# Kernel optimization log

Hardware: AMD Instinct MI355X
Metric: run time of the kernel (lower is better)

## Reference

```python
import jax, jax.numpy as jnp
import numpy as np

D = 256      # d_model (module-level constant in source)
H = 4        # num_heads
HD = D // H  # head dim = 64
B = 16
T = 512
STEP = 0.5   # self.step_size
NEG = -1e9
SCALE = 1.0 / np.sqrt(HD).astype(np.float32)


def _ln(x, g, b):
    m = jnp.mean(x, -1, keepdims=True)
    v = jnp.var(x, -1, keepdims=True)
    return (x - m) / jnp.sqrt(v + 1e-5) * g + b


def _forward(x, h0,
             sa_wq, sa_wk, sa_wv, sa_wo, sa_bq, sa_bk, sa_bv, sa_bo,
             f_w1, f_b1, f_w2, f_b2,
             ta_wq, ta_wk, ta_wv, ta_wo, ta_bq, ta_bk, ta_bv, ta_bo,
             tr_w1, tr_b1, tr_w2, tr_b2,
             ps_w, ps_b, sp_w, sp_b,
             ln1_g, ln1_b, ln2_g, ln2_b, ln3_g, ln3_b, ln4_g, ln4_b):
    Bz, Tz, Dz = x.shape
    # ---- causal self-attention over parallel_repr ----
    q = (x @ sa_wq + sa_bq).reshape(Bz, Tz, H, HD)
    k = (x @ sa_wk + sa_bk).reshape(Bz, Tz, H, HD)
    v = (x @ sa_wv + sa_bv).reshape(Bz, Tz, H, HD)
    scores = jnp.einsum('bqhd,bkhd->bhqk', q, k) * SCALE
    causal = jnp.tril(jnp.ones((Tz, Tz), bool))
    scores = jnp.where(causal, scores, NEG)
    attn = jnp.einsum('bhqk,bkhd->bqhd', jax.nn.softmax(scores, -1), v)
    attn = attn.reshape(Bz, Tz, Dz) @ sa_wo + sa_bo
    x = _ln(x + attn, ln1_g, ln1_b)
    # ---- FFN with sequential guidance ----
    guid = h0 @ sp_w + sp_b                      # sequential_to_parallel, [B, D]
    ffn_in = x + 0.3 * guid[:, None, :]
    ffn = jax.nn.gelu(ffn_in @ f_w1 + f_b1, approximate=False) @ f_w2 + f_b2
    x = _ln(x + ffn, ln2_g, ln2_b)
    # ---- sequential scan with growing-cache trajectory attention ----
    # past states only enter through their K/V projections, so project each
    # new state once when it is appended (same math as re-projecting the cache).
    def step(carry, inp):
        h, kbuf, vbuf = carry                    # kbuf/vbuf: [T, B, H, HD]
        t, xt = inp                              # xt: [B, D]
        qt = (xt @ ta_wq + ta_bq).reshape(Bz, H, HD)
        sc = jnp.einsum('bhd,tbhd->bht', qt, kbuf) * SCALE
        valid = (jnp.arange(Tz) < t)[None, None, :]
        ctx = jnp.einsum('bht,tbhd->bhd',
                         jax.nn.softmax(jnp.where(valid, sc, NEG), -1), vbuf)
        ctx = ctx.reshape(Bz, Dz) @ ta_wo + ta_bo
        ctx = jnp.where(t > 0, ctx, 0.0)         # torch code zeroes context at t=0
        pg = xt @ ps_w + ps_b                    # parallel_to_sequential
        comb = jnp.concatenate([xt + 0.3 * pg, ctx], -1)
        delta = jax.nn.gelu(comb @ tr_w1 + tr_b1, approximate=False) @ tr_w2 + tr_b2
        h = _ln(h + STEP * delta, ln3_g, ln3_b)
        kbuf = kbuf.at[t].set((h @ ta_wk + ta_bk).reshape(Bz, H, HD))
        vbuf = vbuf.at[t].set((h @ ta_wv + ta_bv).reshape(Bz, H, HD))
        return (h, kbuf, vbuf), None

    buf0 = jnp.zeros((Tz, Bz, H, HD), x.dtype)
    (hT, _, _), _ = jax.lax.scan(step, (h0, buf0, buf0),
                                 (jnp.arange(Tz), jnp.swapaxes(x, 0, 1)))
    return x, _ln(hT, ln4_g, ln4_b)


def setup_inputs() -> dict:
    ks = iter(jax.random.split(jax.random.key(0), 64))
    def w(*shape):
        return jax.random.normal(next(ks), shape, jnp.float32) * 0.02
    inp = {
        'x': jax.random.normal(next(ks), (B, T, D), jnp.float32),
        'h0': jax.random.normal(next(ks), (B, D), jnp.float32),
        'sa_wq': w(D, D), 'sa_wk': w(D, D), 'sa_wv': w(D, D), 'sa_wo': w(D, D),
        'sa_bq': w(D), 'sa_bk': w(D), 'sa_bv': w(D), 'sa_bo': w(D),
        'f_w1': w(D, 4 * D), 'f_b1': w(4 * D), 'f_w2': w(4 * D, D), 'f_b2': w(D),
        'ta_wq': w(D, D), 'ta_wk': w(D, D), 'ta_wv': w(D, D), 'ta_wo': w(D, D),
        'ta_bq': w(D), 'ta_bk': w(D), 'ta_bv': w(D), 'ta_bo': w(D),
        'tr_w1': w(2 * D, 2 * D), 'tr_b1': w(2 * D), 'tr_w2': w(2 * D, D), 'tr_b2': w(D),
        'ps_w': w(D, D), 'ps_b': w(D), 'sp_w': w(D, D), 'sp_b': w(D),
        'ln1_g': jnp.ones(D), 'ln1_b': jnp.zeros(D),
        'ln2_g': jnp.ones(D), 'ln2_b': jnp.zeros(D),
        'ln3_g': jnp.ones(D), 'ln3_b': jnp.zeros(D),
        'ln4_g': jnp.ones(D), 'ln4_b': jnp.zeros(D),
    }
    return inp


def reference(x, h0,
              sa_wq, sa_wk, sa_wv, sa_wo, sa_bq, sa_bk, sa_bv, sa_bo,
              f_w1, f_b1, f_w2, f_b2,
              ta_wq, ta_wk, ta_wv, ta_wo, ta_bq, ta_bk, ta_bv, ta_bo,
              tr_w1, tr_b1, tr_w2, tr_b2,
              ps_w, ps_b, sp_w, sp_b,
              ln1_g, ln1_b, ln2_g, ln2_b, ln3_g, ln3_b, ln4_g, ln4_b):
    return _forward(x, h0,
                    sa_wq, sa_wk, sa_wv, sa_wo, sa_bq, sa_bk, sa_bv, sa_bo,
                    f_w1, f_b1, f_w2, f_b2,
                    ta_wq, ta_wk, ta_wv, ta_wo, ta_bq, ta_bk, ta_bv, ta_bo,
                    tr_w1, tr_b1, tr_w2, tr_b2,
                    ps_w, ps_b, sp_w, sp_b,
                    ln1_g, ln1_b, ln2_g, ln2_b, ln3_g, ln3_b, ln4_g, ln4_b)
```

## Files before the change

kernel.cpp:

```cpp
#include <hip/hip_runtime.h>
#include <hip/hip_bf16.h>

typedef __bf16 bf16x8 __attribute__((ext_vector_type(8)));
typedef float f32x4 __attribute__((ext_vector_type(4)));

__device__ __forceinline__ float b2f(ushort u){
  union { uint u; float f; } x; x.u = ((uint)u) << 16; return x.f;
}
__device__ __forceinline__ ushort f2b(float f){
  union { float f; uint u; } x; x.f = f;
  uint r = x.u + 0x7fff + ((x.u >> 16) & 1);
  return (ushort)(r >> 16);
}
__device__ __forceinline__ uint pack_bf2(float a, float b){
  return (uint)f2b(a) | ((uint)f2b(b) << 16);
}
__device__ __forceinline__ float lo16(uint u){ union{uint a;float f;}x; x.a=u<<16; return x.f; }
__device__ __forceinline__ float hi16(uint u){ union{uint a;float f;}x; x.a=u&0xffff0000u; return x.f; }
__device__ __forceinline__ float gelu_exact(float v){
  return 0.5f * v * (1.0f + erff(v * 0.70710678118654752f));
}

template<int AF32, int ACT>
__global__ __launch_bounds__(256) void gemm_kernel(
    const void* __restrict__ Av, const float* __restrict__ W, int ldw,
    const float* __restrict__ bias, const float* residf,
    float* Cf, ushort* Cb,
    int M, int N, int K, float scale)
{
  __shared__ __align__(16) ushort Al[64*40];
  __shared__ __align__(16) ushort Bl[64*40];
  const int nb = N >> 6;
  const int rb = blockIdx.x / nb, cb = blockIdx.x % nb;
  const int tid = threadIdx.x;
  const int w = tid >> 6, l = tid & 63;
  f32x4 acc[4];
#pragma unroll
  for(int i=0;i<4;i++) acc[i] = (f32x4){0.f,0.f,0.f,0.f};
  const int ar = tid >> 2, ai = (tid & 3) << 3;
  const int bk = tid >> 3, bn = (tid & 7) << 3;
  for(int kb = 0; kb < K; kb += 32){
    uint4 au;
    if(AF32){
      const float* Ap = (const float*)Av + (size_t)(rb*64 + ar)*K + kb + ai;
      float4 f0 = *(const float4*)Ap;
      float4 f1 = *(const float4*)(Ap + 4);
      au.x = pack_bf2(f0.x,f0.y); au.y = pack_bf2(f0.z,f0.w);
      au.z = pack_bf2(f1.x,f1.y); au.w = pack_bf2(f1.z,f1.w);
    } else {
      au = *(const uint4*)((const ushort*)Av + (size_t)(rb*64 + ar)*K + kb + ai);
    }
    const float* Wp = W + (size_t)(kb + bk)*ldw + cb*64 + bn;
    float4 w0 = *(const float4*)Wp;
    float4 w1 = *(const float4*)(Wp + 4);
    ushort bs[8];
    bs[0]=f2b(w0.x); bs[1]=f2b(w0.y); bs[2]=f2b(w0.z); bs[3]=f2b(w0.w);
    bs[4]=f2b(w1.x); bs[5]=f2b(w1.y); bs[6]=f2b(w1.z); bs[7]=f2b(w1.w);
    __syncthreads();
    *(uint4*)&Al[ar*40 + ai] = au;
#pragma unroll
    for(int i=0;i<8;i++) Bl[(bn+i)*40 + bk] = bs[i];
    __syncthreads();
    bf16x8 af = *(const bf16x8*)&Al[(w*16 + (l&15))*40 + (l>>4)*8];
#pragma unroll
    for(int c4=0;c4<4;c4++){
      bf16x8 bfv = *(const bf16x8*)&Bl[(c4*16 + (l&15))*40 + (l>>4)*8];
      acc[c4] = __builtin_amdgcn_mfma_f32_16x16x32_bf16(af, bfv, acc[c4], 0,0,0);
    }
  }
#pragma unroll
  for(int c4=0;c4<4;c4++){
#pragma unroll
    for(int r=0;r<4;r++){
      int row = rb*64 + w*16 + (l>>4)*4 + r;
      int col = cb*64 + c4*16 + (l&15);
      size_t idx = (size_t)row*N + col;
      float vv = acc[c4][r];
      if(bias) vv += bias[col];
      vv *= scale;
      if(residf) vv += residf[idx];
      if(ACT) vv = gelu_exact(vv);
      if(Cf) Cf[idx] = vv;
      if(Cb) Cb[idx] = f2b(vv);
    }
  }
}

__global__ __launch_bounds__(256) void attn_kernel(const ushort* __restrict__ Q,
    const ushort* __restrict__ K, const ushort* __restrict__ V, ushort* __restrict__ O)
{
  __shared__ float s[16*520];
  __shared__ float kt[64*66];
  __shared__ float rowm[16], rowr[16], redx[256];
  const int bid = blockIdx.x;
  const int qb = bid & 31, h = (bid>>5)&3, b = bid>>7;
  const int tid = threadIdx.x;
  const int qi = tid >> 4, jj = tid & 15;
  const int qrow = qb*16 + qi;
  float qreg[64];
  {
    const ushort* qp = Q + ((size_t)(b*512 + qrow))*256 + h*64;
#pragma unroll
    for(int d=0; d<64; d++) qreg[d] = b2f(qp[d])*0.125f;
  }
  const int ntile = (qb*16 + 79) >> 6;
  for(int jt=0; jt<ntile; jt++){
    {
      int jr = tid >> 2, d0 = (tid & 3) << 4;
      const ushort* kp = K + ((size_t)(b*512 + jt*64 + jr))*256 + h*64 + d0;
#pragma unroll
      for(int i=0;i<16;i++) kt[jr*66 + d0 + i] = b2f(kp[i]);
    }
    __syncthreads();
#pragma unroll
    for(int jl=0;jl<4;jl++){
      int jloc = jj*4 + jl;
      int j = jt*64 + jloc;
      float a = 0.f;
#pragma unroll
      for(int d=0; d<64; d++) a += qreg[d]*kt[jloc*66 + d];
      s[qi*520 + j] = (j <= qrow) ? a : -1e30f;
    }
    __syncthreads();
  }
  const int nj = ntile*64;
  float m = -1e30f;
  for(int j=jj; j<nj; j+=16) m = fmaxf(m, s[qi*520 + j]);
  redx[jj*16 + qi] = m;
  __syncthreads();
  if(tid < 16){
    float mm = -1e30f;
#pragma unroll
    for(int k2=0;k2<16;k2++) mm = fmaxf(mm, redx[k2*16 + tid]);
    rowm[tid] = mm;
  }
  __syncthreads();
  float mrow = rowm[qi];
  float ssum = 0.f;
  for(int j=jj; j<nj; j+=16){
    float e = __expf(s[qi*520+j] - mrow);
    s[qi*520+j] = e; ssum += e;
  }
  redx[jj*16 + qi] = ssum;
  __syncthreads();
  if(tid < 16){
    float t2 = 0.f;
#pragma unroll
    for(int k2=0;k2<16;k2++) t2 += redx[k2*16 + tid];
    rowr[tid] = 1.0f/t2;
  }
  const int dd = jj;
  float acc4[4] = {0,0,0,0};
  for(int jt=0; jt<ntile; jt++){
    __syncthreads();
    {
      int jr = tid >> 2, d0 = (tid & 3) << 4;
      const ushort* vp = V + ((size_t)(b*512 + jt*64 + jr))*256 + h*64 + d0;
#pragma unroll
      for(int i=0;i<16;i++) kt[jr*66 + d0 + i] = b2f(vp[i]);
    }
    __syncthreads();
#pragma unroll
    for(int jl=0;jl<64;jl++){
      float p = s[qi*520 + jt*64 + jl];
#pragma unroll
      for(int i=0;i<4;i++) acc4[i] += p*kt[jl*66 + dd*4 + i];
    }
  }
  float rr = rowr[qi];
  ushort* op = O + ((size_t)(b*512 + qrow))*256 + h*64 + dd*4;
#pragma unroll
  for(int i=0;i<4;i++) op[i] = f2b(acc4[i]*rr);
}

__global__ __launch_bounds__(256) void ln_kernel(const float* __restrict__ in,
    const float* __restrict__ g, const float* __restrict__ be,
    float* outf, ushort* outb)
{
  int row = blockIdx.x*4 + (threadIdx.x>>6);
  int lane = threadIdx.x & 63;
  size_t idx = (size_t)row*256 + lane*4;
  float4 v = *(const float4*)(in + idx);
  float s1 = v.x+v.y+v.z+v.w;
  float s2 = v.x*v.x + v.y*v.y + v.z*v.z + v.w*v.w;
#pragma unroll
  for(int off=32; off; off>>=1){ s1 += __shfl_xor(s1,off); s2 += __shfl_xor(s2,off); }
  float mu = s1*(1.f/256.f);
  float var = s2*(1.f/256.f) - mu*mu;
  float r = rsqrtf(var + 1e-5f);
  float vals[4] = {v.x,v.y,v.z,v.w};
  float4 o4; ushort4 ob;
  float* oo = (float*)&o4; ushort* obp = (ushort*)&ob;
#pragma unroll
  for(int i=0;i<4;i++){
    int d = lane*4 + i;
    float y = (vals[i]-mu)*r*g[d] + be[d];
    oo[i] = y; obp[i] = f2b(y);
  }
  if(outf) *(float4*)(outf+idx) = o4;
  if(outb) *(ushort4*)(outb+idx) = ob;
}

__global__ void guid_kernel(const float* __restrict__ h0, const float* __restrict__ spw,
                            const float* __restrict__ spb, float* __restrict__ guid)
{
  int b = blockIdx.x, c = threadIdx.x;
  float s = spb[c];
  for(int r=0;r<256;r++) s += h0[b*256+r]*spw[r*256+c];
  guid[b*256+c] = s;
}

__global__ void ffnin_kernel(const float* __restrict__ x1, const float* __restrict__ guid,
                             ushort* __restrict__ out)
{
  size_t base = ((size_t)blockIdx.x*256 + threadIdx.x)*8;
  int row = (int)(base >> 8); int bb = row >> 9; int c = (int)(base & 255);
  float4 v0 = *(const float4*)(x1 + base);
  float4 v1 = *(const float4*)(x1 + base + 4);
  const float* gp = guid + bb*256 + c;
  const float* xs = (const float*)&v0;
  ushort o[8];
#pragma unroll
  for(int i=0;i<4;i++) o[i] = f2b(xs[i] + 0.3f*gp[i]);
  const float* xs1 = (const float*)&v1;
#pragma unroll
  for(int i=0;i<4;i++) o[4+i] = f2b(xs1[i] + 0.3f*gp[4+i]);
  *(uint4*)(out + base) = *(uint4*)o;
}

__global__ void bo_kernel(const float* __restrict__ ta_bo, const float* __restrict__ tr_w1,
                          float* __restrict__ bo_f)
{
  int c = threadIdx.x;
  float s = 0.f;
  for(int m=0;m<256;m++) s += ta_bo[m]*tr_w1[(size_t)(256+m)*512 + c];
  bo_f[c] = s;
}

__global__ __launch_bounds__(512, 1) void scan_kernel(
    const ushort* __restrict__ qtb, const ushort* __restrict__ Ubf,
    const float* __restrict__ Wf, const float* __restrict__ bo_f,
    float* cbuf, float* dbuf, int* flags,
    const float* __restrict__ ta_wk, const float* __restrict__ ta_wv,
    const float* __restrict__ ta_bk, const float* __restrict__ ta_bv,
    const float* __restrict__ tr_w2, const float* __restrict__ tr_b2,
    const float* __restrict__ ln3_g, const float* __restrict__ ln3_b,
    const float* __restrict__ ln4_g, const float* __restrict__ ln4_b,
    const float* __restrict__ h0, float* __restrict__ out_h)
{
  __shared__ __align__(16) float red[2][1024];
  __shared__ __align__(16) float pbuf[512];
  __shared__ __align__(16) float hbuf[256];
  __shared__ __align__(16) float ctxL[256];
  __shared__ __align__(16) float qbufS[2][64];
  __shared__ float mG[2][16], sG[2][16];
  __shared__ __align__(16) float numS[2][64];
  __shared__ float mzS[2][2];
  __shared__ float sLastP[4];
  __shared__ __align__(16) float glbuf[128];
  __shared__ int cp_same[4];
  extern __shared__ __align__(16) ushort dynL[];
  ushort* kcL = dynL;
  ushort* vcL = dynL + 512*66;

  const int tid = threadIdx.x;
  const int bid = blockIdx.x;
  const int b = bid & 15;
  const int role = bid >> 4;
  const int b4 = b*4;
  const int w8 = tid >> 6;

  if(role < 4){
    for(int i = tid; i < 512*66; i += 512){ kcL[i] = 0; vcL[i] = 0; }
  }

  int myxcc;
  asm volatile("s_getreg_b32 %0, hwreg(HW_REG_XCC_ID)" : "=s"(myxcc));
  if(tid == 0)
    __hip_atomic_store(&flags[256 + bid], myxcc + 1, __ATOMIC_RELEASE, __HIP_MEMORY_SCOPE_AGENT);
  if(tid < 4){
    int cbid = (role < 4) ? (64 + tid*16 + b) : (tid*16 + b);
    int v;
    while((v = __hip_atomic_load(&flags[256 + cbid], __ATOMIC_ACQUIRE, __HIP_MEMORY_SCOPE_AGENT)) == 0)
      __builtin_amdgcn_s_sleep(8);
    cp_same[tid] = ((v - 1) == myxcc);
  }
  __syncthreads();
  const int anyrem = !(cp_same[0] && cp_same[1] && cp_same[2] && cp_same[3]);

  if(role < 4){
    const int hd = role;
    const int bh = b4 + hd;
    const int out = tid >> 2, sX = tid & 3;
    const int kvSel = out >> 6, colX = out & 63;
    const float* WX = kvSel ? ta_wv : ta_wk;
    uint wp[32];
#pragma unroll
    for(int i=0;i<32;i++){
      int r0 = 8*i + 2*sX;
      wp[i] = pack_bf2(WX[(size_t)r0*256 + hd*64 + colX],
                       WX[(size_t)(r0+1)*256 + hd*64 + colX]);
    }
    const float pbX = kvSel ? ta_bv[hd*64 + colX] : ta_bk[hd*64 + colX];
    float h4[4], b2r4[4], g34[4], b34[4];
    if(tid < 64){
#pragma unroll
      for(int c=0;c<4;c++){
        int d = 4*tid + c;
        h4[c] = h0[b*256 + d]; b2r4[c] = tr_b2[d]; g34[c] = ln3_g[d]; b34[c] = ln3_b[d];
      }
      *(float4*)&hbuf[4*tid] = *(float4*)h4;
    }
    const int j_sh = (tid >= 64) ? (tid - 64) : (448 + tid);
    const int gsh = j_sh >> 5;
    const int lsh = tid & 31;
    __syncthreads();

    ushort qpre = 0;
    if(tid >= 448) qpre = qtb[((size_t)(b*512 + 1))*256 + hd*64 + (tid - 448)];

#pragma clang loop unroll(disable)
    for(int t=0;t<512;t++){
      if(tid >= 448){
        qbufS[(t+1)&1][tid-448] = b2f(qpre)*0.125f;
        int tq = (t+2 < 512) ? (t+2) : 511;
        qpre = qtb[((size_t)(b*512 + tq))*256 + hd*64 + (tid - 448)];
      }
      if(t > 0){
        float acc = 0.f;
#pragma unroll
        for(int i=0;i<32;i++){
          float2 hv = *(const float2*)&hbuf[8*i + 2*sX];
          acc += hv.x*lo16(wp[i]) + hv.y*hi16(wp[i]);
        }
        acc += __shfl_xor(acc, 1);
        acc += __shfl_xor(acc, 2);
        float kf = acc + pbX;
        if(sX == 0){
          ushort u = f2b(kf);
          if(kvSel == 0) kcL[(t-1)*66 + colX] = u;
          else           vcL[(t-1)*66 + colX] = u;
        }
        float pv = (kvSel == 0 && sX == 0) ? qbufS[t&1][colX]*kf : 0.f;
        pv += __shfl_xor(pv, 4);
        pv += __shfl_xor(pv, 8);
        pv += __shfl_xor(pv, 16);
        pv += __shfl_xor(pv, 32);
        if(tid < 256 && (tid & 63) == 0) sLastP[tid >> 6] = pv;
        __syncthreads();
        if(tid < 64){
          const int par = t & 1;
          float sl = (sLastP[0] + sLastP[1]) + (sLastP[2] + sLastP[3]);
          float mo = mzS[par][0], Zo = mzS[par][1];
          float m = fmaxf(mo, sl);
          float so = __expf(mo - m);
          float el = __expf(sl - m);
          float Z = Zo*so + el;
          float vlast = b2f(vcL[(t-1)*66 + tid]);
          cbuf[b*256 + hd*64 + tid] = (numS[par][tid]*so + el*vlast) / Z;
          asm volatile("s_waitcnt vmcnt(0)" ::: "memory");
          if(tid == 0){
            *(volatile int*)&flags[bh] = t;
            if(anyrem)
              __hip_atomic_store(&flags[128 + bh], t, __ATOMIC_RELEASE, __HIP_MEMORY_SCOPE_AGENT);
          }
        }
      }

      {
        const int par = (t+1)&1;
        float s = -3.0e38f;
        if(j_sh < t){
          const uint* kr = (const uint*)(kcL + j_sh*66);
          const float* qS = qbufS[par];
          float a = 0.f;
#pragma unroll
          for(int w=0; w<32; w++){
            uint kk = kr[w];
            float2 q2 = *(const float2*)&qS[2*w];
            a += q2.x*lo16(kk) + q2.y*hi16(kk);
          }
          s = a;
        }
        float gm = s;
#pragma unroll
        for(int off=16; off; off>>=1) gm = fmaxf(gm, __shfl_xor(gm, off));
        float e = (j_sh < t) ? __expf(s - gm) : 0.f;
        pbuf[j_sh] = e;
        float gs = e;
#pragma unroll
        for(int off=16; off; off>>=1) gs += __shfl_xor(gs, off);
        if(lsh == 0){ mG[par][gsh] = gm; sG[par][gsh] = gs; }
        int nn = t - gsh*32; nn = nn < 0 ? 0 : (nn > 32 ? 32 : nn);
        float a0 = 0.f, a1 = 0.f;
        const uint* vbase = (const uint*)vcL;
#pragma unroll 4
        for(int i=0;i<nn;i++){
          int j2 = gsh*32 + i;
          uint vv = vbase[j2*33 + lsh];
          float p = pbuf[j2];
          a0 += p*lo16(vv); a1 += p*hi16(vv);
        }
        float2 pr; pr.x = a0; pr.y = a1;
        *(float2*)&red[par][gsh*64 + 2*lsh] = pr;
      }
      __syncthreads();
      if(tid < 64){
        const int par = (t+1)&1;
        float mo = mG[par][0];
#pragma unroll
        for(int g=1; g<16; g++) mo = fmaxf(mo, mG[par][g]);
        float Zo = 0.f, nm = 0.f;
#pragma unroll
        for(int g=0; g<16; g++){
          float scl = __expf(mG[par][g] - mo);
          Zo += sG[par][g]*scl;
          nm += red[par][g*64 + tid]*scl;
        }
        numS[par][tid] = nm;
        if(tid == 0){ mzS[par][0] = mo; mzS[par][1] = Zo; }
      }
      if(tid < 32){
        const int sh = tid >> 3, wv = tid & 7;
        if(cp_same[sh]){
          while(*(volatile int*)&flags[512 + (b4+sh)*8 + wv] < t+1) __builtin_amdgcn_s_sleep(1);
        } else {
          while(__hip_atomic_load(&flags[1024 + (b4+sh)*8 + wv], __ATOMIC_RELAXED, __HIP_MEMORY_SCOPE_AGENT) < t+1)
            __builtin_amdgcn_s_sleep(2);
        }
      }
      if(tid < 64){
        if(anyrem) __builtin_amdgcn_fence(__ATOMIC_ACQUIRE, "agent");
        float ds[4] = {0.f,0.f,0.f,0.f};
#pragma unroll
        for(int i=0;i<4;i++){
          const float* dp = &dbuf[(b4+i)*256 + 4*tid];
#pragma unroll
          for(int c=0;c<4;c++)
            ds[c] += __hip_atomic_load(dp + c, __ATOMIC_RELAXED, __HIP_MEMORY_SCOPE_AGENT);
        }
        float v4[4]; float s1 = 0.f, s2 = 0.f;
#pragma unroll
        for(int c=0;c<4;c++){
          v4[c] = h4[c] + 0.5f*(ds[c] + b2r4[c]);
          s1 += v4[c]; s2 += v4[c]*v4[c];
        }
#pragma unroll
        for(int off=32; off; off>>=1){ s1 += __shfl_xor(s1,off); s2 += __shfl_xor(s2,off); }
        float mu = s1*(1.f/256.f);
        float qq = s2*(1.f/256.f) - mu*mu;
        float rstd = rsqrtf(qq + 1e-5f);
#pragma unroll
        for(int c=0;c<4;c++) h4[c] = (v4[c]-mu)*rstd*g34[c] + b34[c];
        *(float4*)&hbuf[4*tid] = *(float4*)h4;
      }
      __syncthreads();
    }

    if(hd == 0 && tid < 64){
      float s1 = 0.f, s2 = 0.f;
#pragma unroll
      for(int c=0;c<4;c++){ s1 += h4[c]; s2 += h4[c]*h4[c]; }
#pragma unroll
      for(int off=32; off; off>>=1){ s1 += __shfl_xor(s1,off); s2 += __shfl_xor(s2,off); }
      float mu = s1*(1.f/256.f);
      float qq = s2*(1.f/256.f) - mu*mu;
      float rstd = rsqrtf(qq + 1e-5f);
#pragma unroll
      for(int c=0;c<4;c++){
        int d = 4*tid + c;
        out_h[b*256 + d] = (h4[c]-mu)*rstd*ln4_g[d] + ln4_b[d];
      }
    }
  } else {
    const int ish = role - 4;
    const int hid = tid >> 2, sY = tid & 3;
    const int colY = ish*128 + hid;
    uint wfp[32];
#pragma unroll
    for(int i=0;i<32;i++){
      int r0 = 8*i + 2*sY;
      wfp[i] = pack_bf2(Wf[(size_t)r0*512 + colY], Wf[(size_t)(r0+1)*512 + colY]);
    }
    const int dcol = tid >> 1, s2 = tid & 1;
    uint w2p[32];
#pragma unroll
    for(int i=0;i<32;i++){
      int r0 = ish*128 + 4*i + 2*s2;
      w2p[i] = pack_bf2(tr_w2[(size_t)r0*256 + dcol], tr_w2[(size_t)(r0+1)*256 + dcol]);
    }
    const float borr = (sY==0) ? bo_f[colY] : 0.f;
    __syncthreads();

#pragma clang loop unroll(disable)
    for(int t=0;t<512;t++){
      ushort uvs = 0;
      if(sY == 0) uvs = Ubf[((size_t)(b*512 + t))*512 + colY];
      if(t > 0){
        if(tid < 256){
          int q = tid >> 6;
          if(cp_same[q]){
            while(*(volatile int*)&flags[b4 + q] < t) __builtin_amdgcn_s_sleep(1);
          } else {
            while(__hip_atomic_load(&flags[128 + b4 + q], __ATOMIC_RELAXED, __HIP_MEMORY_SCOPE_AGENT) < t)
              __builtin_amdgcn_s_sleep(2);
          }
        }
        if(anyrem) __builtin_amdgcn_fence(__ATOMIC_ACQUIRE, "agent");
        if(tid < 256) ctxL[tid] = *(volatile float*)&cbuf[b*256 + tid];
      }
      __syncthreads();
      float accf = 0.f;
      if(t > 0){
#pragma unroll
        for(int i=0;i<32;i++){
          float2 c2 = *(const float2*)&ctxL[8*i + 2*sY];
          accf += c2.x*lo16(wfp[i]) + c2.y*hi16(wfp[i]);
        }
        accf += __shfl_xor(accf, 1);
        accf += __shfl_xor(accf, 2);
      }
      if(sY == 0){
        float g1 = b2f(uvs) + ((t>0) ? (borr + accf) : 0.f);
        glbuf[hid] = gelu_exact(g1);
      }
      __syncthreads();
      {
        float dp = 0.f;
#pragma unroll
        for(int i=0;i<32;i++){
          float2 gv = *(const float2*)&glbuf[4*i + 2*s2];
          dp += gv.x*lo16(w2p[i]) + gv.y*hi16(w2p[i]);
        }
        dp += __shfl_xor(dp, 1);
        if(s2 == 0) dbuf[(b4+ish)*256 + dcol] = dp;
      }
      asm volatile("s_waitcnt vmcnt(0)" ::: "memory");
      if((tid & 63) == 0){
        *(volatile int*)&flags[512 + (b4+ish)*8 + w8] = t+1;
        if(anyrem)
          __hip_atomic_store(&flags[1024 + (b4+ish)*8 + w8], t+1, __ATOMIC_RELEASE, __HIP_MEMORY_SCOPE_AGENT);
      }
    }
  }
}

#define OFF_FLAGS ((size_t)0)
#define OFF_BOF   ((size_t)8192)
#define OFF_CBUF  ((size_t)16384)
#define OFF_DBUF  ((size_t)32768)
#define OFF_GUID  ((size_t)98304)
#define OFF_WF    ((size_t)131072)
#define OFF_Z1    ((size_t)(1u<<20))
#define OFF_Z2    ((size_t)(5u<<20))
#define OFF_Z3    ((size_t)(9u<<20))
#define OFF_Z4    ((size_t)(13u<<20))
#define OFF_M     ((size_t)(17u<<20))

#define SCAN_DYN_LDS (512*66*2*2)

extern "C" void kernel_launch(void* const* d_in, const int* in_sizes, int n_in,
                              void* d_out, int out_size, void* d_ws, size_t ws_size,
                              hipStream_t stream)
{
  const float* x     = (const float*)d_in[0];
  const float* h0    = (const float*)d_in[1];
  const float* sa_wq = (const float*)d_in[2];
  const float* sa_wk = (const float*)d_in[3];
  const float* sa_wv = (const float*)d_in[4];
  const float* sa_wo = (const float*)d_in[5];
  const float* sa_bq = (const float*)d_in[6];
  const float* sa_bk = (const float*)d_in[7];
  const float* sa_bv = (const float*)d_in[8];
  const float* sa_bo = (const float*)d_in[9];
  const float* f_w1  = (const float*)d_in[10];
  const float* f_b1  = (const float*)d_in[11];
  const float* f_w2  = (const float*)d_in[12];
  const float* f_b2  = (const float*)d_in[13];
  const float* ta_wq = (const float*)d_in[14];
  const float* ta_wk = (const float*)d_in[15];
  const float* ta_wv = (const float*)d_in[16];
  const float* ta_wo = (const float*)d_in[17];
  const float* ta_bq = (const float*)d_in[18];
  const float* ta_bk = (const float*)d_in[19];
  const float* ta_bv = (const float*)d_in[20];
  const float* ta_bo = (const float*)d_in[21];
  const float* tr_w1 = (const float*)d_in[22];
  const float* tr_b1 = (const float*)d_in[23];
  const float* tr_w2 = (const float*)d_in[24];
  const float* tr_b2 = (const float*)d_in[25];
  const float* ps_w  = (const float*)d_in[26];
  const float* ps_b  = (const float*)d_in[27];
  const float* sp_w  = (const float*)d_in[28];
  const float* sp_b  = (const float*)d_in[29];
  const float* ln1_g = (const float*)d_in[30];
  const float* ln1_b = (const float*)d_in[31];
  const float* ln2_g = (const float*)d_in[32];
  const float* ln2_b = (const float*)d_in[33];
  const float* ln3_g = (const float*)d_in[34];
  const float* ln3_b = (const float*)d_in[35];
  const float* ln4_g = (const float*)d_in[36];
  const float* ln4_b = (const float*)d_in[37];

  char* ws = (char*)d_ws;
  int*    flags = (int*)   (ws + OFF_FLAGS);
  float*  bo_f  = (float*) (ws + OFF_BOF);
  float*  cbuf  = (float*) (ws + OFF_CBUF);
  float*  dbuf  = (float*) (ws + OFF_DBUF);
  float*  guid  = (float*) (ws + OFF_GUID);
  float*  Wff   = (float*) (ws + OFF_WF);
  ushort* qb    = (ushort*)(ws + OFF_Z1);
  ushort* kb    = (ushort*)(ws + OFF_Z2);
  ushort* vb    = (ushort*)(ws + OFF_Z3);
  ushort* attnb = (ushort*)(ws + OFF_Z4);
  float*  x0pre = (float*) (ws + OFF_Z1);
  float*  x1f   = (float*) (ws + OFF_Z3);
  ushort* ffnb  = (ushort*)(ws + OFF_M);
  ushort* mid   = (ushort*)(ws + OFF_M + (4u<<20));
  float*  x2pre = (float*) (ws + OFF_Z1);
  ushort* abf   = (ushort*)(ws + OFF_Z4);
  ushort* qtb   = (ushort*)(ws + OFF_Z3);
  ushort* Ubf   = (ushort*)(ws + OFF_M);
  float*  outb  = (float*)d_out;
  float*  out_h = outb + (out_size - 4096);

  static int attr_done = 0;
  if(!attr_done){
    hipFuncSetAttribute((const void*)scan_kernel,
                        hipFuncAttributeMaxDynamicSharedMemorySize, SCAN_DYN_LDS);
    attr_done = 1;
  }

  hipMemsetAsync(flags, 0, 8192, stream);

  gemm_kernel<1,0><<<512, 256, 0, stream>>>(x, sa_wq, 256, sa_bq, nullptr, nullptr, qb, 8192,256,256, 1.0f);
  gemm_kernel<1,0><<<512, 256, 0, stream>>>(x, sa_wk, 256, sa_bk, nullptr, nullptr, kb, 8192,256,256, 1.0f);
  gemm_kernel<1,0><<<512, 256, 0, stream>>>(x, sa_wv, 256, sa_bv, nullptr, nullptr, vb, 8192,256,256, 1.0f);
  attn_kernel<<<2048, 256, 0, stream>>>(qb, kb, vb, attnb);
  gemm_kernel<0,0><<<512, 256, 0, stream>>>(attnb, sa_wo, 256, sa_bo, x, x0pre, nullptr, 8192,256,256, 1.0f);
  ln_kernel<<<2048, 256, 0, stream>>>(x0pre, ln1_g, ln1_b, x1f, nullptr);
  guid_kernel<<<16, 256, 0, stream>>>(h0, sp_w, sp_b, guid);
  ffnin_kernel<<<1024, 256, 0, stream>>>(x1f, guid, ffnb);
  gemm_kernel<0,1><<<1024, 256, 0, stream>>>(ffnb, f_w1, 1024, f_b1, nullptr, nullptr, mid, 8192,512,256, 1.0f);
  gemm_kernel<0,0><<<512, 256, 0, stream>>>(mid, f_w2, 256, f_b2, x1f, x2pre, nullptr, 8192,256,512, 1.0f);
  gemm_kernel<0,1><<<1024, 256, 0, stream>>>(ffnb, f_w1 + 512, 1024, f_b1 + 512, nullptr, nullptr, mid, 8192,512,256, 1.0f);
  gemm_kernel<0,0><<<512, 256, 0, stream>>>(mid, f_w2 + (size_t)512*256, 256, nullptr, x2pre, x2pre, nullptr, 8192,256,512, 1.0f);
  ln_kernel<<<2048, 256, 0, stream>>>(x2pre, ln2_g, ln2_b, outb, nullptr);

  gemm_kernel<1,0><<<512, 256, 0, stream>>>(outb, ps_w, 256, ps_b, outb, nullptr, abf, 8192,256,256, 0.3f);
  gemm_kernel<0,0><<<1024, 256, 0, stream>>>(abf, tr_w1, 512, tr_b1, nullptr, nullptr, Ubf, 8192,512,256, 1.0f);
  gemm_kernel<1,0><<<512, 256, 0, stream>>>(outb, ta_wq, 256, ta_bq, nullptr, nullptr, qtb, 8192,256,256, 1.0f);
  gemm_kernel<1,0><<<32, 256, 0, stream>>>(ta_wo, tr_w1 + (size_t)256*512, 512, nullptr, nullptr, Wff, nullptr, 256,512,256, 1.0f);
  bo_kernel<<<1, 512, 0, stream>>>(ta_bo, tr_w1, bo_f);

  scan_kernel<<<128, 512, SCAN_DYN_LDS, stream>>>(qtb, Ubf, Wff, bo_f, cbuf, dbuf, flags,
                                                  ta_wk, ta_wv, ta_bk, ta_bv, tr_w2, tr_b2,
                                                  ln3_g, ln3_b, ln4_g, ln4_b, h0, out_h);
}
```

Before: 3.526 ms.

## Pack data with step tags to replace separate flag handshakes in scan

The cross-block handshakes in the sequential scan kernel are rebuilt. Each value now goes out as a 64-bit word holding the data and the step index as a float, so consumers poll the data itself instead of waiting on a separate flag and then reading the payload. This removes the vmcnt waits, the flag stores and the acquire fences from the per-step critical path. The dot-product loops are also split into four independent accumulators for more instruction-level parallelism. In exchange, the cbuf and dbuf buffers double in size, the memset grows, and correctness now depends on 64-bit stores being atomic.

```diff
diff --git a/kernel.cpp b/kernel.cpp
--- a/kernel.cpp
+++ b/kernel.cpp
@@ -20,6 +20,8 @@
 __device__ __forceinline__ float gelu_exact(float v){
   return 0.5f * v * (1.0f + erff(v * 0.70710678118654752f));
 }
+
+union U64F2 { unsigned long long u; float2 f; };
 
 template<int AF32, int ACT>
 __global__ __launch_bounds__(256) void gemm_kernel(
@@ -240,7 +242,7 @@
 __global__ __launch_bounds__(512, 1) void scan_kernel(
     const ushort* __restrict__ qtb, const ushort* __restrict__ Ubf,
     const float* __restrict__ Wf, const float* __restrict__ bo_f,
-    float* cbuf, float* dbuf, int* flags,
+    float2* cbuf, float2* dbuf, int* flags,
     const float* __restrict__ ta_wk, const float* __restrict__ ta_wv,
     const float* __restrict__ ta_bk, const float* __restrict__ ta_bv,
     const float* __restrict__ tr_w2, const float* __restrict__ tr_b2,
@@ -268,7 +270,6 @@
   const int b = bid & 15;
   const int role = bid >> 4;
   const int b4 = b*4;
-  const int w8 = tid >> 6;
 
   if(role < 4){
     for(int i = tid; i < 512*66; i += 512){ kcL[i] = 0; vcL[i] = 0; }
@@ -290,7 +291,6 @@
 
   if(role < 4){
     const int hd = role;
-    const int bh = b4 + hd;
     const int out = tid >> 2, sX = tid & 3;
     const int kvSel = out >> 6, colX = out & 63;
     const float* WX = kvSel ? ta_wv : ta_wk;
@@ -327,12 +327,19 @@
         qpre = qtb[((size_t)(b*512 + tq))*256 + hd*64 + (tid - 448)];
       }
       if(t > 0){
-        float acc = 0.f;
-#pragma unroll
-        for(int i=0;i<32;i++){
-          float2 hv = *(const float2*)&hbuf[8*i + 2*sX];
-          acc += hv.x*lo16(wp[i]) + hv.y*hi16(wp[i]);
-        }
+        float aa0=0.f, aa1=0.f, aa2=0.f, aa3=0.f;
+#pragma unroll
+        for(int i=0;i<32;i+=4){
+          float2 h0v = *(const float2*)&hbuf[8*i + 2*sX];
+          float2 h1v = *(const float2*)&hbuf[8*(i+1) + 2*sX];
+          float2 h2v = *(const float2*)&hbuf[8*(i+2) + 2*sX];
+          float2 h3v = *(const float2*)&hbuf[8*(i+3) + 2*sX];
+          aa0 += h0v.x*lo16(wp[i])   + h0v.y*hi16(wp[i]);
+          aa1 += h1v.x*lo16(wp[i+1]) + h1v.y*hi16(wp[i+1]);
+          aa2 += h2v.x*lo16(wp[i+2]) + h2v.y*hi16(wp[i+2]);
+          aa3 += h3v.x*lo16(wp[i+3]) + h3v.y*hi16(wp[i+3]);
+        }
+        float acc = (aa0+aa1)+(aa2+aa3);
         acc += __shfl_xor(acc, 1);
         acc += __shfl_xor(acc, 2);
         float kf = acc + pbX;
@@ -357,13 +364,10 @@
           float el = __expf(sl - m);
           float Z = Zo*so + el;
           float vlast = b2f(vcL[(t-1)*66 + tid]);
-          cbuf[b*256 + hd*64 + tid] = (numS[par][tid]*so + el*vlast) / Z;
-          asm volatile("s_waitcnt vmcnt(0)" ::: "memory");
-          if(tid == 0){
-            *(volatile int*)&flags[bh] = t;
-            if(anyrem)
-              __hip_atomic_store(&flags[128 + bh], t, __ATOMIC_RELEASE, __HIP_MEMORY_SCOPE_AGENT);
-          }
+          U64F2 st; st.f.x = (numS[par][tid]*so + el*vlast) / Z; st.f.y = (float)t;
+          unsigned long long* cp = (unsigned long long*)&cbuf[b*256 + hd*64 + tid];
+          if(!anyrem) *(volatile unsigned long long*)cp = st.u;
+          else __hip_atomic_store(cp, st.u, __ATOMIC_RELEASE, __HIP_MEMORY_SCOPE_AGENT);
         }
       }
 
@@ -373,14 +377,20 @@
         if(j_sh < t){
           const uint* kr = (const uint*)(kcL + j_sh*66);
           const float* qS = qbufS[par];
-          float a = 0.f;
-#pragma unroll
-          for(int w=0; w<32; w++){
-            uint kk = kr[w];
-            float2 q2 = *(const float2*)&qS[2*w];
-            a += q2.x*lo16(kk) + q2.y*hi16(kk);
+          float a0=0.f, a1=0.f, a2=0.f, a3=0.f;
+#pragma unroll
+          for(int w=0; w<32; w+=4){
+            uint k0 = kr[w], k1 = kr[w+1], k2 = kr[w+2], k3 = kr[w+3];
+            float2 q0 = *(const float2*)&qS[2*w];
+            float2 q1 = *(const float2*)&qS[2*(w+1)];
+            float2 q2 = *(const float2*)&qS[2*(w+2)];
+            float2 q3 = *(const float2*)&qS[2*(w+3)];
+            a0 += q0.x*lo16(k0) + q0.y*hi16(k0);
+            a1 += q1.x*lo16(k1) + q1.y*hi16(k1);
+            a2 += q2.x*lo16(k2) + q2.y*hi16(k2);
+            a3 += q3.x*lo16(k3) + q3.y*hi16(k3);
           }
-          s = a;
+          s = (a0+a1)+(a2+a3);
         }
         float gm = s;
 #pragma unroll
@@ -407,38 +417,59 @@
       __syncthreads();
       if(tid < 64){
         const int par = (t+1)&1;
-        float mo = mG[par][0];
-#pragma unroll
-        for(int g=1; g<16; g++) mo = fmaxf(mo, mG[par][g]);
-        float Zo = 0.f, nm = 0.f;
-#pragma unroll
-        for(int g=0; g<16; g++){
-          float scl = __expf(mG[par][g] - mo);
-          Zo += sG[par][g]*scl;
-          nm += red[par][g*64 + tid]*scl;
-        }
-        numS[par][tid] = nm;
-        if(tid == 0){ mzS[par][0] = mo; mzS[par][1] = Zo; }
-      }
-      if(tid < 32){
-        const int sh = tid >> 3, wv = tid & 7;
-        if(cp_same[sh]){
-          while(*(volatile int*)&flags[512 + (b4+sh)*8 + wv] < t+1) __builtin_amdgcn_s_sleep(1);
+        float m0 = mG[par][0], m1 = mG[par][1];
+#pragma unroll
+        for(int g=2; g<16; g+=2){ m0 = fmaxf(m0, mG[par][g]); m1 = fmaxf(m1, mG[par][g+1]); }
+        float mo = fmaxf(m0, m1);
+        float Zo0=0.f, Zo1=0.f, nm0=0.f, nm1=0.f;
+#pragma unroll
+        for(int g=0; g<16; g+=2){
+          float sc0 = __expf(mG[par][g] - mo);
+          float sc1 = __expf(mG[par][g+1] - mo);
+          Zo0 += sG[par][g]*sc0;   Zo1 += sG[par][g+1]*sc1;
+          nm0 += red[par][g*64 + tid]*sc0;
+          nm1 += red[par][(g+1)*64 + tid]*sc1;
+        }
+        numS[par][tid] = nm0 + nm1;
+        if(tid == 0){ mzS[par][0] = mo; mzS[par][1] = Zo0 + Zo1; }
+      }
+      if(tid < 64){
+        float ds[4] = {0.f,0.f,0.f,0.f};
+        const float want = (float)(t+1);
+        U64F2 xx[16];
+        if(!anyrem){
+          int ok;
+          do{
+            ok = 1;
+#pragma unroll
+            for(int i=0;i<4;i++)
+#pragma unroll
+              for(int c=0;c<4;c++)
+                xx[i*4+c].u = *(volatile unsigned long long*)&dbuf[(b4+i)*256 + 4*tid + c];
+#pragma unroll
+            for(int k2=0;k2<16;k2++) ok &= (xx[k2].f.y == want);
+          } while(!ok);
         } else {
-          while(__hip_atomic_load(&flags[1024 + (b4+sh)*8 + wv], __ATOMIC_RELAXED, __HIP_MEMORY_SCOPE_AGENT) < t+1)
-            __builtin_amdgcn_s_sleep(2);
-        }
-      }
-      if(tid < 64){
-        if(anyrem) __builtin_amdgcn_fence(__ATOMIC_ACQUIRE, "agent");
-        float ds[4] = {0.f,0.f,0.f,0.f};
-#pragma unroll
-        for(int i=0;i<4;i++){
-          const float* dp = &dbuf[(b4+i)*256 + 4*tid];
-#pragma unroll
-          for(int c=0;c<4;c++)
-            ds[c] += __hip_atomic_load(dp + c, __ATOMIC_RELAXED, __HIP_MEMORY_SCOPE_AGENT);
-        }
+          int ok;
+          do{
+            ok = 1;
+#pragma unroll
+            for(int i=0;i<4;i++)
+#pragma unroll
+              for(int c=0;c<4;c++){
+                unsigned long long* pp = (unsigned long long*)&dbuf[(b4+i)*256 + 4*tid + c];
+                xx[i*4+c].u = cp_same[i] ? *(volatile unsigned long long*)pp
+                    : __hip_atomic_load(pp, __ATOMIC_RELAXED, __HIP_MEMORY_SCOPE_AGENT);
+              }
+#pragma unroll
+            for(int k2=0;k2<16;k2++) ok &= (xx[k2].f.y == want);
+            if(!ok) __builtin_amdgcn_s_sleep(1);
+          } while(!ok);
+        }
+#pragma unroll
+        for(int i=0;i<4;i++)
+#pragma unroll
+          for(int c=0;c<4;c++) ds[c] += xx[i*4+c].f.x;
         float v4[4]; float s1 = 0.f, s2 = 0.f;
 #pragma unroll
         for(int c=0;c<4;c++){
@@ -498,25 +529,38 @@
       if(sY == 0) uvs = Ubf[((size_t)(b*512 + t))*512 + colY];
       if(t > 0){
         if(tid < 256){
-          int q = tid >> 6;
+          const int q = tid >> 6;
+          unsigned long long* sp = (unsigned long long*)&cbuf[b*256 + tid];
+          U64F2 x;
+          const float tf = (float)t;
           if(cp_same[q]){
-            while(*(volatile int*)&flags[b4 + q] < t) __builtin_amdgcn_s_sleep(1);
+            do { x.u = *(volatile unsigned long long*)sp; } while(x.f.y != tf);
           } else {
-            while(__hip_atomic_load(&flags[128 + b4 + q], __ATOMIC_RELAXED, __HIP_MEMORY_SCOPE_AGENT) < t)
-              __builtin_amdgcn_s_sleep(2);
+            for(;;){
+              x.u = __hip_atomic_load(sp, __ATOMIC_RELAXED, __HIP_MEMORY_SCOPE_AGENT);
+              if(x.f.y == tf) break;
+              __builtin_amdgcn_s_sleep(1);
+            }
           }
-        }
-        if(anyrem) __builtin_amdgcn_fence(__ATOMIC_ACQUIRE, "agent");
-        if(tid < 256) ctxL[tid] = *(volatile float*)&cbuf[b*256 + tid];
+          ctxL[tid] = x.f.x;
+        }
       }
       __syncthreads();
       float accf = 0.f;
       if(t > 0){
-#pragma unroll
-        for(int i=0;i<32;i++){
-          float2 c2 = *(const float2*)&ctxL[8*i + 2*sY];
-          accf += c2.x*lo16(wfp[i]) + c2.y*hi16(wfp[i]);
-        }
+        float aa0=0.f, aa1=0.f, aa2=0.f, aa3=0.f;
+#pragma unroll
+        for(int i=0;i<32;i+=4){
+          float2 c0 = *(const float2*)&ctxL[8*i + 2*sY];
+          float2 c1 = *(const float2*)&ctxL[8*(i+1) + 2*sY];
+          float2 c2 = *(const float2*)&ctxL[8*(i+2) + 2*sY];
+          float2 c3 = *(const float2*)&ctxL[8*(i+3) + 2*sY];
+          aa0 += c0.x*lo16(wfp[i])   + c0.y*hi16(wfp[i]);
+          aa1 += c1.x*lo16(wfp[i+1]) + c1.y*hi16(wfp[i+1]);
+          aa2 += c2.x*lo16(wfp[i+2]) + c2.y*hi16(wfp[i+2]);
+          aa3 += c3.x*lo16(wfp[i+3]) + c3.y*hi16(wfp[i+3]);
+        }
+        accf = (aa0+aa1)+(aa2+aa3);
         accf += __shfl_xor(accf, 1);
         accf += __shfl_xor(accf, 2);
       }
@@ -526,20 +570,26 @@
       }
       __syncthreads();
       {
-        float dp = 0.f;
-#pragma unroll
-        for(int i=0;i<32;i++){
-          float2 gv = *(const float2*)&glbuf[4*i + 2*s2];
-          dp += gv.x*lo16(w2p[i]) + gv.y*hi16(w2p[i]);
-        }
+        float aa0=0.f, aa1=0.f, aa2=0.f, aa3=0.f;
+#pragma unroll
+        for(int i=0;i<32;i+=4){
+          float2 g0 = *(const float2*)&glbuf[4*i + 2*s2];
+          float2 g1v = *(const float2*)&glbuf[4*(i+1) + 2*s2];
+          float2 g2 = *(const float2*)&glbuf[4*(i+2) + 2*s2];
+          float2 g3 = *(const float2*)&glbuf[4*(i+3) + 2*s2];
+          aa0 += g0.x*lo16(w2p[i])    + g0.y*hi16(w2p[i]);
+          aa1 += g1v.x*lo16(w2p[i+1]) + g1v.y*hi16(w2p[i+1]);
+          aa2 += g2.x*lo16(w2p[i+2])  + g2.y*hi16(w2p[i+2]);
+          aa3 += g3.x*lo16(w2p[i+3])  + g3.y*hi16(w2p[i+3]);
+        }
+        float dp = (aa0+aa1)+(aa2+aa3);
         dp += __shfl_xor(dp, 1);
-        if(s2 == 0) dbuf[(b4+ish)*256 + dcol] = dp;
-      }
-      asm volatile("s_waitcnt vmcnt(0)" ::: "memory");
-      if((tid & 63) == 0){
-        *(volatile int*)&flags[512 + (b4+ish)*8 + w8] = t+1;
-        if(anyrem)
-          __hip_atomic_store(&flags[1024 + (b4+ish)*8 + w8], t+1, __ATOMIC_RELEASE, __HIP_MEMORY_SCOPE_AGENT);
+        if(s2 == 0){
+          U64F2 st; st.f.x = dp; st.f.y = (float)(t+1);
+          unsigned long long* pp = (unsigned long long*)&dbuf[(b4+ish)*256 + dcol];
+          if(!anyrem) *(volatile unsigned long long*)pp = st.u;
+          else __hip_atomic_store(pp, st.u, __ATOMIC_RELEASE, __HIP_MEMORY_SCOPE_AGENT);
+        }
       }
     }
   }
@@ -548,9 +598,9 @@
 #define OFF_FLAGS ((size_t)0)
 #define OFF_BOF   ((size_t)8192)
 #define OFF_CBUF  ((size_t)16384)
-#define OFF_DBUF  ((size_t)32768)
-#define OFF_GUID  ((size_t)98304)
-#define OFF_WF    ((size_t)131072)
+#define OFF_DBUF  ((size_t)49152)
+#define OFF_GUID  ((size_t)180224)
+#define OFF_WF    ((size_t)196608)
 #define OFF_Z1    ((size_t)(1u<<20))
 #define OFF_Z2    ((size_t)(5u<<20))
 #define OFF_Z3    ((size_t)(9u<<20))
@@ -605,8 +655,8 @@
   char* ws = (char*)d_ws;
   int*    flags = (int*)   (ws + OFF_FLAGS);
   float*  bo_f  = (float*) (ws + OFF_BOF);
-  float*  cbuf  = (float*) (ws + OFF_CBUF);
-  float*  dbuf  = (float*) (ws + OFF_DBUF);
+  float2* cbuf  = (float2*)(ws + OFF_CBUF);
+  float2* dbuf  = (float2*)(ws + OFF_DBUF);
   float*  guid  = (float*) (ws + OFF_GUID);
   float*  Wff   = (float*) (ws + OFF_WF);
   ushort* qb    = (ushort*)(ws + OFF_Z1);
@@ -631,7 +681,7 @@
     attr_done = 1;
   }
 
-  hipMemsetAsync(flags, 0, 8192, stream);
+  hipMemsetAsync(ws, 0, OFF_GUID, stream);
 
   gemm_kernel<1,0><<<512, 256, 0, stream>>>(x, sa_wq, 256, sa_bq, nullptr, nullptr, qb, 8192,256,256, 1.0f);
   gemm_kernel<1,0><<<512, 256, 0, stream>>>(x, sa_wk, 256, sa_bk, nullptr, nullptr, kb, 8192,256,256, 1.0f);
```

New measurement: 3.981 ms. +12.9%, slower.
